# Optimization experiments

Hardware: AMD Instinct MI355X
Metric: run time of the kernel (lower is better)

## Reference

```python
import jax, jax.numpy as jnp
import numpy as np

IN_DIM, OUT_DIM, HID = 32, 1, 256
H0, H1, H2 = HID // 4, HID // 2, HID
B, S = 256, 512


def setup_inputs() -> dict:
    key = jax.random.key(0)
    ks = jax.random.split(key, 16)

    def u(k, shape, fan):
        bound = 1.0 / np.sqrt(fan)
        return jax.random.uniform(k, shape, jnp.float32, -bound, bound)

    inp = {"noise": jax.random.normal(ks[0], (B, S, IN_DIM), jnp.float32)}
    dims = [(IN_DIM, H0), (H0, H1), (H1, H2)]
    for i, (din, h) in enumerate(dims):
        inp[f"Wih{i}"] = u(ks[1 + 4 * i], (4 * h, din), h)  # torch gate order i,f,g,o
        inp[f"Whh{i}"] = u(ks[2 + 4 * i], (4 * h, h), h)
        inp[f"bih{i}"] = u(ks[3 + 4 * i], (4 * h,), h)
        inp[f"bhh{i}"] = u(ks[4 + 4 * i], (4 * h,), h)
    inp["Wl"] = u(ks[13], (OUT_DIM, H2), H2)
    inp["bl"] = u(ks[14], (OUT_DIM,), H2)
    return inp


def lstm_layer(x, Wih, Whh, bih, bhh):
    # x: [B, S, D] -> hidden sequence [B, S, H]; zero initial (h, c), torch gate order i,f,g,o
    Bb = x.shape[0]
    H = Whh.shape[1]
    pre = jnp.einsum('bsd,gd->bsg', x, Wih) + bih + bhh  # input GEMM for all timesteps at once

    def step(carry, pre_t):
        h, c = carry
        g = pre_t + h @ Whh.T  # [B, 4H]
        i, f, gg, o = jnp.split(g, 4, axis=-1)
        c = jax.nn.sigmoid(f) * c + jax.nn.sigmoid(i) * jnp.tanh(gg)
        h = jax.nn.sigmoid(o) * jnp.tanh(c)
        return (h, c), h

    h0 = jnp.zeros((Bb, H), x.dtype)
    c0 = jnp.zeros((Bb, H), x.dtype)
    _, hs = jax.lax.scan(step, (h0, c0), jnp.swapaxes(pre, 0, 1))  # scan over time
    return jnp.swapaxes(hs, 0, 1)


def reference(noise, Wih0, Whh0, bih0, bhh0, Wih1, Whh1, bih1, bhh1,
              Wih2, Whh2, bih2, bhh2, Wl, bl):
    x = lstm_layer(noise, Wih0, Whh0, bih0, bhh0)   # [B, S, 64]
    x = lstm_layer(x, Wih1, Whh1, bih1, bhh1)        # [B, S, 128]
    x = lstm_layer(x, Wih2, Whh2, bih2, bhh2)        # [B, S, 256]
    return jnp.tanh(jnp.einsum('bsh,oh->bso', x, Wl) + bl)  # [B, S, OUT_DIM]
```

## Files before the change

kernel.cpp:

```cpp
#include <hip/hip_runtime.h>
#include <hip/hip_fp16.h>

#define DEVINL __device__ __forceinline__

constexpr int B = 256, S = 512;
constexpr int H0 = 64, H1 = 128, H2 = 256;

typedef _Float16 f16x8 __attribute__((ext_vector_type(8)));
typedef float f32x4 __attribute__((ext_vector_type(4)));
typedef _Float16 h2v __attribute__((ext_vector_type(2)));

DEVINL float fexp2(float x) { return __builtin_amdgcn_exp2f(x); }
DEVINL float frcp(float x) { return __builtin_amdgcn_rcpf(x); }
DEVINL float fsig(float x) { return frcp(1.f + fexp2(-1.44269504088896f * x)); }
DEVINL float ftanh_(float x) { return 1.f - 2.f * frcp(1.f + fexp2(2.88539008177793f * x)); }
DEVINL h2v as_h2(unsigned u) { union { unsigned u; h2v h; } x; x.u = u; return x.h; }
DEVINL float fdot2(unsigned a, unsigned b, float c) {
  return __builtin_amdgcn_fdot2(as_h2(a), as_h2(b), c, false);
}
union FU { uint4 u; f16x8 h; };
DEVINL f16x8 as_f16x8(uint4 u) { FU x; x.u = u; return x.h; }

DEVINL unsigned long long agldull(unsigned long long* p) {
  return __hip_atomic_load(p, __ATOMIC_RELAXED, __HIP_MEMORY_SCOPE_AGENT);
}
DEVINL void agstull(unsigned long long* p, unsigned long long v) {
  __hip_atomic_store(p, v, __ATOMIC_RELAXED, __HIP_MEMORY_SCOPE_AGENT);
}


__global__ __launch_bounds__(256) void pack_frag(const float* __restrict__ w,
    uint4* __restrict__ wp, int Hch, int Kdim, int MT, int KT) {
  int o = blockIdx.x * 256 + threadIdx.x;
  if (o >= MT * KT * 64) return;
  int lane = o & 63, fk = o >> 6;
  int kt = fk % KT, mt = fk / KT;
  int rp = mt * 16 + (lane & 15);
  int orig = (rp & 3) * Hch + (rp >> 2);
  int k0 = kt * 32 + (lane >> 4) * 8;
  unsigned r[4];
#pragma unroll
  for (int p = 0; p < 4; ++p) {
    unsigned lo = __half_as_ushort(__float2half_rn(w[(size_t)orig * Kdim + k0 + 2 * p]));
    unsigned hi = __half_as_ushort(__float2half_rn(w[(size_t)orig * Kdim + k0 + 2 * p + 1]));
    r[p] = lo | (hi << 16);
  }
  uint4 v; v.x = r[0]; v.y = r[1]; v.z = r[2]; v.w = r[3];
  wp[o] = v;
}

__global__ __launch_bounds__(256) void pack_bias(const float* __restrict__ bih,
    const float* __restrict__ bhh, float* __restrict__ bs, int Hch) {
  int rp = blockIdx.x * 256 + threadIdx.x;
  if (rp >= 4 * Hch) return;
  int orig = (rp & 3) * Hch + (rp >> 2);
  bs[rp] = bih[orig] + bhh[orig];
}

__global__ void pack_wl(const float* __restrict__ wl, unsigned* __restrict__ wlp, int n) {
  int i = threadIdx.x;
  if (i < n) {
    unsigned lo = __half_as_ushort(__float2half_rn(wl[2 * i]));
    unsigned hi = __half_as_ushort(__float2half_rn(wl[2 * i + 1]));
    wlp[i] = lo | (hi << 16);
  }
}

__global__ __launch_bounds__(256) void f2h(const float* __restrict__ x,
                                           __half* __restrict__ y, int n8) {
  int i = blockIdx.x * 256 + threadIdx.x;
  if (i >= n8) return;
  float4 a = *(const float4*)(x + i * 8);
  float4 b = *(const float4*)(x + i * 8 + 4);
  __half h[8];
  h[0] = __float2half_rn(a.x); h[1] = __float2half_rn(a.y);
  h[2] = __float2half_rn(a.z); h[3] = __float2half_rn(a.w);
  h[4] = __float2half_rn(b.x); h[5] = __float2half_rn(b.y);
  h[6] = __float2half_rn(b.z); h[7] = __float2half_rn(b.w);
  *(uint4*)(y + i * 8) = *(const uint4*)h;
}

#define KBLK(BUF, K0, K1)                                                           \
  _Pragma("unroll") for (int kt = (K0); kt < (K1); ++kt) {                          \
    f16x8 bfrag = as_f16x8(*(const uint4*)((BUF) + n16 * HP + kt * 32 + quad * 8)); \
    _Pragma("unroll") for (int im = 0; im < MTW; ++im)                              \
      acc[im] = __builtin_amdgcn_mfma_f32_16x16x32_f16(                             \
          as_f16x8(areg[im][kt]), bfrag, acc[im], 0, 0, 0);                         \
  }

template <int H, int SPLIT, bool FINAL, int KTI>
DEVINL void scan_body(
    int bx, const __half* x, const uint4* wpI, const float* bs,
    const uint4* wp, f32x4* preT, __half* xout, float* out,
    const unsigned* wlp, const float* blp,
    float* sth, float* stc, unsigned long long* xh,
    int Sc, int t0, int first) {
  constexpr int MT = H / 4;
  constexpr int MTO = MT / SPLIT;
  constexpr int MTW = MTO / 8;
  constexpr int KT = H / 32;
  constexpr int HP = H + 8;
  constexpr int CH_OWN = MTO * 4;
  constexpr int KI = KTI * 32;

  __shared__ __half hb[2][16 * HP];
  __shared__ unsigned wls[FINAL ? H / 2 : 1];

  const int tid = threadIdx.x, w = tid >> 6, lane = tid & 63;
  const int n16 = lane & 15, quad = lane >> 4;
  int bt, half;
  if constexpr (SPLIT == 2) { bt = bx & 15; half = bx >> 4; }
  else { bt = bx; half = 0; }
  const int b0 = bt * 16;
  const int mbase = half * MTO;

  if constexpr (SPLIT == 2) {
    uint4 wih[MTW][KTI];
#pragma unroll
    for (int im = 0; im < MTW; ++im)
#pragma unroll
      for (int kt = 0; kt < KTI; ++kt)
        wih[im][kt] = wpI[((size_t)(mbase + w * MTW + im) * KTI + kt) * 64 + lane];
    f32x4 bini[MTW];
#pragma unroll
    for (int im = 0; im < MTW; ++im)
      bini[im] = *(const f32x4*)(bs + (mbase + w * MTW + im) * 16 + quad * 4);
    uint4 bfr[KTI];
    {
      const __half* xr = x + ((size_t)(b0 + n16) * S + t0) * KI + quad * 8;
#pragma unroll
      for (int kt = 0; kt < KTI; ++kt) bfr[kt] = *(const uint4*)(xr + kt * 32);
    }
    for (int t = 0; t < Sc; ++t) {
      uint4 cur[KTI];
#pragma unroll
      for (int kt = 0; kt < KTI; ++kt) cur[kt] = bfr[kt];
      if (t + 1 < Sc) {
        const __half* xr = x + ((size_t)(b0 + n16) * S + t0 + t + 1) * KI + quad * 8;
#pragma unroll
        for (int kt = 0; kt < KTI; ++kt) bfr[kt] = *(const uint4*)(xr + kt * 32);
      }
      f32x4 ac[MTW];
#pragma unroll
      for (int im = 0; im < MTW; ++im) ac[im] = bini[im];
#pragma unroll
      for (int kt = 0; kt < KTI; ++kt)
#pragma unroll
        for (int im = 0; im < MTW; ++im)
          ac[im] = __builtin_amdgcn_mfma_f32_16x16x32_f16(as_f16x8(wih[im][kt]),
                                                          as_f16x8(cur[kt]), ac[im], 0, 0, 0);
#pragma unroll
      for (int im = 0; im < MTW; ++im)
        preT[((size_t)(bt * Sc + t) * MT + mbase + w * MTW + im) * 64 + lane] = ac[im];
    }
    asm volatile("s_waitcnt vmcnt(0)" ::: "memory");
  }

  uint4 wih1[SPLIT == 1 ? MTW : 1][SPLIT == 1 ? KTI : 1];
  f32x4 bini1[SPLIT == 1 ? MTW : 1];
  if constexpr (SPLIT == 1) {
#pragma unroll
    for (int im = 0; im < MTW; ++im)
#pragma unroll
      for (int kt = 0; kt < KTI; ++kt)
        wih1[im][kt] = wpI[((size_t)(w * MTW + im) * KTI + kt) * 64 + lane];
#pragma unroll
    for (int im = 0; im < MTW; ++im)
      bini1[im] = *(const f32x4*)(bs + (w * MTW + im) * 16 + quad * 4);
  }

  uint4 areg[MTW][KT];
#pragma unroll
  for (int im = 0; im < MTW; ++im)
#pragma unroll
    for (int kt = 0; kt < KT; ++kt)
      areg[im][kt] = wp[((size_t)(mbase + w * MTW + im) * KT + kt) * 64 + lane];

  if constexpr (FINAL)
    for (int i = tid; i < H / 2; i += 512) wls[i] = wlp[i];

  float cst[MTW];
#pragma unroll
  for (int im = 0; im < MTW; ++im) {
    int ch = (mbase + w * MTW + im) * 4 + quad;
    cst[im] = first ? 0.f : stc[(size_t)(b0 + n16) * H + ch];
  }
  for (int i = tid; i < 16 * H; i += 512) {
    int n = i / H, ch = i % H;
    hb[0][n * HP + ch] = first ? __float2half_rn(0.f)
                               : __float2half_rn(sth[(size_t)(b0 + n) * H + ch]);
  }
  __syncthreads();

  const float bl0 = FINAL ? blp[0] : 0.f;

  auto emit_out = [&](const __half* rbuf, int t_out) {
    if constexpr (FINAL) {
      if ((SPLIT == 1 || half == 0) && tid < 128) {
        int n = tid >> 3, seg = tid & 7;
        const unsigned* hrow = (const unsigned*)(rbuf + n * HP);
        float s = 0.f;
#pragma unroll
        for (int p = 0; p < 16; ++p) s = fdot2(hrow[seg * 16 + p], wls[seg * 16 + p], s);
        s += __shfl_xor(s, 1); s += __shfl_xor(s, 2); s += __shfl_xor(s, 4);
        if (seg == 0) out[(size_t)(b0 + n) * S + t_out] = ftanh_(s + bl0);
      }
    } else {
      if (tid < 16 * (H / 8)) {
        int n = tid / (H / 8), kq = tid % (H / 8);
        uint4 v = *(const uint4*)(rbuf + n * HP + kq * 8);
        *(uint4*)(xout + ((size_t)(b0 + n) * S + t_out) * H + kq * 8) = v;
      }
    }
  };

  f32x4 nxt[MTW];
  if constexpr (SPLIT == 2) {
#pragma unroll
    for (int im = 0; im < MTW; ++im)
      nxt[im] = preT[((size_t)(bt * Sc) * MT + mbase + w * MTW + im) * 64 + lane];
  }
  uint4 xcur[SPLIT == 1 ? KTI : 1];
  if constexpr (SPLIT == 1) {
    const __half* xr = x + ((size_t)(b0 + n16) * S + t0) * KI + quad * 8;
#pragma unroll
    for (int kt = 0; kt < KTI; ++kt) xcur[kt] = *(const uint4*)(xr + kt * 32);
  }

  unsigned long long v0 = 0, v1 = 0;
  const int j0 = w * 128 + lane;

  for (int tl = 0; tl < Sc; ++tl) {
    __half* rb = hb[tl & 1];
    __half* wb = hb[(tl + 1) & 1];
    const int hid = t0 + tl;
    f32x4 acc[MTW];

    if constexpr (SPLIT == 2) {
#pragma unroll
      for (int im = 0; im < MTW; ++im) acc[im] = nxt[im];
      if (tl + 1 < Sc) {
#pragma unroll
        for (int im = 0; im < MTW; ++im)
          nxt[im] = preT[((size_t)(bt * Sc + tl + 1) * MT + mbase + w * MTW + im) * 64 + lane];
      }

      if (half == 0) { KBLK(rb, 0, KT / 2) } else { KBLK(rb, KT / 2, KT) }
      if (tl > 0) {
        const unsigned seq = (unsigned)hid;
        unsigned long long* srcp =
            xh + (((size_t)((hid - 1) & 1) * 16 + bt) * 2 + (1 - half)) * 1024;
        for (;;) {
          bool ok = ((unsigned)(v0 >> 32) == seq) & ((unsigned)(v1 >> 32) == seq);
          if (__all(ok)) break;
          v0 = agldull(srcp + j0);
          v1 = agldull(srcp + j0 + 64);
        }
        int c0 = j0 >> 3, dn0 = j0 & 7;
        rb[(2 * dn0) * HP + (1 - half) * CH_OWN + c0] =
            __ushort_as_half((unsigned short)(v0 & 0xffffu));
        rb[(2 * dn0 + 1) * HP + (1 - half) * CH_OWN + c0] =
            __ushort_as_half((unsigned short)((v0 >> 16) & 0xffffu));
        int j1 = j0 + 64, c1 = j1 >> 3, dn1 = j1 & 7;
        rb[(2 * dn1) * HP + (1 - half) * CH_OWN + c1] =
            __ushort_as_half((unsigned short)(v1 & 0xffffu));
        rb[(2 * dn1 + 1) * HP + (1 - half) * CH_OWN + c1] =
            __ushort_as_half((unsigned short)((v1 >> 16) & 0xffffu));
        __syncthreads();
      }
      if (half == 0) { KBLK(rb, KT / 2, KT) } else { KBLK(rb, 0, KT / 2) }
      if (tl > 0) emit_out(rb, hid - 1);
    } else {
      uint4 xnxt[KTI];
      if (tl + 1 < Sc) {
        const __half* xr = x + ((size_t)(b0 + n16) * S + hid + 1) * KI + quad * 8;
#pragma unroll
        for (int kt = 0; kt < KTI; ++kt) xnxt[kt] = *(const uint4*)(xr + kt * 32);
      }
#pragma unroll
      for (int im = 0; im < MTW; ++im) acc[im] = bini1[im];
#pragma unroll
      for (int kt = 0; kt < KTI; ++kt)
#pragma unroll
        for (int im = 0; im < MTW; ++im)
          acc[im] = __builtin_amdgcn_mfma_f32_16x16x32_f16(as_f16x8(wih1[im][kt]),
                                                           as_f16x8(xcur[kt]), acc[im], 0, 0, 0);
      if (tl > 0) emit_out(rb, hid - 1);
      KBLK(rb, 0, KT)
      if (tl + 1 < Sc) {
#pragma unroll
        for (int kt = 0; kt < KTI; ++kt) xcur[kt] = xnxt[kt];
      }
    }

    __half hh[MTW];
#pragma unroll
    for (int im = 0; im < MTW; ++im) {
      float gi = fsig(acc[im][0]);
      float gf = fsig(acc[im][1]);
      float gg = ftanh_(acc[im][2]);
      float go = fsig(acc[im][3]);
      float cn = gf * cst[im] + gi * gg;
      cst[im] = cn;
      hh[im] = __float2half_rn(go * ftanh_(cn));
    }

    if constexpr (SPLIT == 2) {
      const unsigned eseq = (unsigned)(hid + 1);
      unsigned long long* dst =
          xh + (((size_t)(hid & 1) * 16 + bt) * 2 + half) * 1024;
#pragma unroll
      for (int im = 0; im < MTW; ++im) {
        unsigned m = (unsigned)__half_as_ushort(hh[im]);
        unsigned o = (unsigned)__shfl_xor((int)m, 1);
        if (!(lane & 1)) {
          int cl = (w * MTW + im) * 4 + quad;
          agstull(dst + cl * 8 + (n16 >> 1),
                  ((unsigned long long)eseq << 32) | (unsigned long long)(m | (o << 16)));
        }
      }
      {
        unsigned long long* srcn =
            xh + (((size_t)(hid & 1) * 16 + bt) * 2 + (1 - half)) * 1024;
        v0 = agldull(srcn + j0);
        v1 = agldull(srcn + j0 + 64);
      }
#pragma unroll
      for (int im = 0; im < MTW; ++im)
        wb[n16 * HP + (mbase + w * MTW + im) * 4 + quad] = hh[im];
      __syncthreads();
    } else {
#pragma unroll
      for (int im = 0; im < MTW; ++im)
        wb[n16 * HP + (w * MTW + im) * 4 + quad] = hh[im];
      __syncthreads();
    }
  }

  __half* fb = hb[Sc & 1];
  if constexpr (SPLIT == 2) {
    const unsigned seq = (unsigned)(t0 + Sc);
    unsigned long long* srcp =
        xh + (((size_t)((t0 + Sc - 1) & 1) * 16 + bt) * 2 + (1 - half)) * 1024;
    for (;;) {
      bool ok = ((unsigned)(v0 >> 32) == seq) & ((unsigned)(v1 >> 32) == seq);
      if (__all(ok)) break;
      v0 = agldull(srcp + j0);
      v1 = agldull(srcp + j0 + 64);
    }
    int c0 = j0 >> 3, dn0 = j0 & 7;
    fb[(2 * dn0) * HP + (1 - half) * CH_OWN + c0] =
        __ushort_as_half((unsigned short)(v0 & 0xffffu));
    fb[(2 * dn0 + 1) * HP + (1 - half) * CH_OWN + c0] =
        __ushort_as_half((unsigned short)((v0 >> 16) & 0xffffu));
    int j1 = j0 + 64, c1 = j1 >> 3, dn1 = j1 & 7;
    fb[(2 * dn1) * HP + (1 - half) * CH_OWN + c1] =
        __ushort_as_half((unsigned short)(v1 & 0xffffu));
    fb[(2 * dn1 + 1) * HP + (1 - half) * CH_OWN + c1] =
        __ushort_as_half((unsigned short)((v1 >> 16) & 0xffffu));
    __syncthreads();
  }

  emit_out(fb, t0 + Sc - 1);

  for (int i = tid; i < 16 * H; i += 512) {
    int n = i / H, ch = i % H;
    sth[(size_t)(b0 + n) * H + ch] = __half2float(fb[n * HP + ch]);
  }
#pragma unroll
  for (int im = 0; im < MTW; ++im) {
    int ch = (mbase + w * MTW + im) * 4 + quad;
    stc[(size_t)(b0 + n16) * H + ch] = cst[im];
  }
}
#undef KBLK

__global__ __launch_bounds__(512) void scan_fat(
    const __half* x0, __half* x1, __half* x2,
    const uint4* wpI0, const uint4* wpI1, const uint4* wpI2,
    const float* bs0, const float* bs1, const float* bs2,
    const uint4* wpH0, const uint4* wpH1, const uint4* wpH2,
    f32x4* preT2,
    float* out, const unsigned* wlp, const float* blp,
    float* sh0, float* sc0, float* sh1, float* sc1, float* sh2, float* sc2,
    unsigned long long* xh, int Sc, int slot, int NC) {
  int b = blockIdx.x;
  if (b < 16) {
    int c = slot;
    if (c >= NC) return;
    scan_body<64, 1, false, 1>(b, x0, wpI0, bs0, wpH0, nullptr, x1, nullptr,
                               nullptr, nullptr, sh0, sc0, nullptr, Sc, c * Sc, c == 0);
  } else if (b < 32) {
    int c = slot - 1;
    if (c < 0 || c >= NC) return;
    scan_body<128, 1, false, 2>(b - 16, x1, wpI1, bs1, wpH1, nullptr, x2, nullptr,
                                nullptr, nullptr, sh1, sc1, nullptr, Sc, c * Sc, c == 0);
  } else {
    int c = slot - 2;
    if (c < 0 || c >= NC) return;
    scan_body<256, 2, true, 4>(b - 32, x2, wpI2, bs2, wpH2, preT2, nullptr, out,
                               wlp, blp, sh2, sc2, xh, Sc, c * Sc, c == 0);
  }
}

extern "C" void kernel_launch(void* const* d_in, const int* in_sizes, int n_in,
                              void* d_out, int out_size, void* d_ws, size_t ws_size,
                              hipStream_t stream) {
  (void)in_sizes; (void)n_in; (void)out_size;
  const float* noise = (const float*)d_in[0];
  const float* Wih0 = (const float*)d_in[1];
  const float* Whh0 = (const float*)d_in[2];
  const float* bih0 = (const float*)d_in[3];
  const float* bhh0 = (const float*)d_in[4];
  const float* Wih1 = (const float*)d_in[5];
  const float* Whh1 = (const float*)d_in[6];
  const float* bih1 = (const float*)d_in[7];
  const float* bhh1 = (const float*)d_in[8];
  const float* Wih2 = (const float*)d_in[9];
  const float* Whh2 = (const float*)d_in[10];
  const float* bih2 = (const float*)d_in[11];
  const float* bhh2 = (const float*)d_in[12];
  const float* Wl = (const float*)d_in[13];
  const float* bl = (const float*)d_in[14];
  float* out = (float*)d_out;

  char* p = (char*)d_ws;
  auto alloc = [&](size_t bytes) {
    char* r = p;
    p += (bytes + 255) & ~(size_t)255;
    return r;
  };
  uint4* wpH0 = (uint4*)alloc((size_t)16 * 2 * 1024);
  uint4* wpH1 = (uint4*)alloc((size_t)32 * 4 * 1024);
  uint4* wpH2 = (uint4*)alloc((size_t)64 * 8 * 1024);
  uint4* wpI0 = (uint4*)alloc((size_t)16 * 1 * 1024);
  uint4* wpI1 = (uint4*)alloc((size_t)32 * 2 * 1024);
  uint4* wpI2 = (uint4*)alloc((size_t)64 * 4 * 1024);
  float* bs0 = (float*)alloc(256 * 4);
  float* bs1 = (float*)alloc(512 * 4);
  float* bs2 = (float*)alloc(1024 * 4);
  unsigned* wlp = (unsigned*)alloc(128 * 4);
  float* sh0 = (float*)alloc((size_t)B * H0 * 4);
  float* sc0 = (float*)alloc((size_t)B * H0 * 4);
  float* sh1 = (float*)alloc((size_t)B * H1 * 4);
  float* sc1 = (float*)alloc((size_t)B * H1 * 4);
  float* sh2 = (float*)alloc((size_t)B * H2 * 4);
  float* sc2 = (float*)alloc((size_t)B * H2 * 4);
  __half* x0 = (__half*)alloc((size_t)B * S * 32 * 2);
  __half* x1 = (__half*)alloc((size_t)B * S * H0 * 2);
  __half* x2 = (__half*)alloc((size_t)B * S * H1 * 2);
  unsigned long long* xh = (unsigned long long*)alloc((size_t)2 * 16 * 2 * 1024 * 8);
  size_t fixed = (size_t)(p - (char*)d_ws);
  int Sc = 64;
  while (Sc > 16 && fixed + (size_t)B * Sc * 16 * H2 > ws_size) Sc >>= 1;
  f32x4* preT2 = (f32x4*)alloc((size_t)B * Sc * 16 * H2);

  hipMemsetAsync(xh, 0, (size_t)2 * 16 * 2 * 1024 * 8, stream);

  pack_frag<<<(16 * 2 * 64 + 255) / 256, 256, 0, stream>>>(Whh0, wpH0, 64, 64, 16, 2);
  pack_frag<<<(32 * 4 * 64 + 255) / 256, 256, 0, stream>>>(Whh1, wpH1, 128, 128, 32, 4);
  pack_frag<<<(64 * 8 * 64 + 255) / 256, 256, 0, stream>>>(Whh2, wpH2, 256, 256, 64, 8);
  pack_frag<<<(16 * 1 * 64 + 255) / 256, 256, 0, stream>>>(Wih0, wpI0, 64, 32, 16, 1);
  pack_frag<<<(32 * 2 * 64 + 255) / 256, 256, 0, stream>>>(Wih1, wpI1, 128, 64, 32, 2);
  pack_frag<<<(64 * 4 * 64 + 255) / 256, 256, 0, stream>>>(Wih2, wpI2, 256, 128, 64, 4);
  pack_bias<<<1, 256, 0, stream>>>(bih0, bhh0, bs0, 64);
  pack_bias<<<2, 256, 0, stream>>>(bih1, bhh1, bs1, 128);
  pack_bias<<<4, 256, 0, stream>>>(bih2, bhh2, bs2, 256);
  pack_wl<<<1, 128, 0, stream>>>(Wl, wlp, 128);
  f2h<<<(B * S * 32 / 8 + 255) / 256, 256, 0, stream>>>(noise, x0, B * S * 32 / 8);

  int NC = S / Sc;
  for (int slot = 0; slot < NC + 2; ++slot)
    scan_fat<<<64, 512, 0, stream>>>(x0, x1, x2, wpI0, wpI1, wpI2, bs0, bs1, bs2,
                                     wpH0, wpH1, wpH2, preT2,
                                     out, wlp, bl, sh0, sc0, sh1, sc1, sh2, sc2,
                                     xh, Sc, slot, NC);
}
```

Before: 1.924 ms.

## Duplicate cross-block hidden-state exchange via L2 atomics and split final projection

The exchange of hidden-state halves between the paired layer-2 blocks is now written to two buffers. One uses the existing agent-scope relaxed store, the other uses a workgroup-scope atomic exchange that may resolve at L2 faster. The consumer polls both and accepts whichever carries the expected sequence tag. The final output projection is also split so each half-block computes 8 of the 16 batch rows instead of one block doing all 16. This doubles exchange traffic and polling loads, and relies on workgroup-scope atomics being visible across blocks, which is not guaranteed by the memory model.

```diff
diff --git a/kernel.cpp b/kernel.cpp
--- a/kernel.cpp
+++ b/kernel.cpp
@@ -26,6 +26,12 @@
 }
 DEVINL void agstull(unsigned long long* p, unsigned long long v) {
   __hip_atomic_store(p, v, __ATOMIC_RELAXED, __HIP_MEMORY_SCOPE_AGENT);
+}
+DEVINL unsigned long long l2ldull(unsigned long long* p) {
+  return __hip_atomic_fetch_add(p, 0ull, __ATOMIC_RELAXED, __HIP_MEMORY_SCOPE_WORKGROUP);
+}
+DEVINL void l2stull(unsigned long long* p, unsigned long long v) {
+  (void)__hip_atomic_exchange(p, v, __ATOMIC_RELAXED, __HIP_MEMORY_SCOPE_WORKGROUP);
 }
 
 
@@ -93,7 +99,7 @@
     int bx, const __half* x, const uint4* wpI, const float* bs,
     const uint4* wp, f32x4* preT, __half* xout, float* out,
     const unsigned* wlp, const float* blp,
-    float* sth, float* stc, unsigned long long* xh,
+    float* sth, float* stc, unsigned long long* xhA, unsigned long long* xhF,
     int Sc, int t0, int first) {
   constexpr int MT = H / 4;
   constexpr int MTO = MT / SPLIT;
@@ -196,14 +202,29 @@
 
   auto emit_out = [&](const __half* rbuf, int t_out) {
     if constexpr (FINAL) {
-      if ((SPLIT == 1 || half == 0) && tid < 128) {
-        int n = tid >> 3, seg = tid & 7;
+      if (tid < 64) {
+        int n = (tid >> 3) + (SPLIT == 2 ? half * 8 : 0);
+        int seg = tid & 7;
         const unsigned* hrow = (const unsigned*)(rbuf + n * HP);
         float s = 0.f;
 #pragma unroll
         for (int p = 0; p < 16; ++p) s = fdot2(hrow[seg * 16 + p], wls[seg * 16 + p], s);
         s += __shfl_xor(s, 1); s += __shfl_xor(s, 2); s += __shfl_xor(s, 4);
         if (seg == 0) out[(size_t)(b0 + n) * S + t_out] = ftanh_(s + bl0);
+        if constexpr (SPLIT == 1) {
+        }
+      }
+      if constexpr (SPLIT == 1) {
+        if (tid >= 64 && tid < 128) {
+          int n = (tid >> 3);
+          int seg = tid & 7;
+          const unsigned* hrow = (const unsigned*)(rbuf + n * HP);
+          float s = 0.f;
+#pragma unroll
+          for (int p = 0; p < 16; ++p) s = fdot2(hrow[seg * 16 + p], wls[seg * 16 + p], s);
+          s += __shfl_xor(s, 1); s += __shfl_xor(s, 2); s += __shfl_xor(s, 4);
+          if (seg == 0) out[(size_t)(b0 + n) * S + t_out] = ftanh_(s + bl0);
+        }
       }
     } else {
       if (tid < 16 * (H / 8)) {
@@ -227,7 +248,7 @@
     for (int kt = 0; kt < KTI; ++kt) xcur[kt] = *(const uint4*)(xr + kt * 32);
   }
 
-  unsigned long long v0 = 0, v1 = 0;
+  unsigned long long v0f = 0, v1f = 0, v0a = 0, v1a = 0;
   const int j0 = w * 128 + lane;
 
   for (int tl = 0; tl < Sc; ++tl) {
@@ -248,24 +269,30 @@
       if (half == 0) { KBLK(rb, 0, KT / 2) } else { KBLK(rb, KT / 2, KT) }
       if (tl > 0) {
         const unsigned seq = (unsigned)hid;
-        unsigned long long* srcp =
-            xh + (((size_t)((hid - 1) & 1) * 16 + bt) * 2 + (1 - half)) * 1024;
+        const size_t so = (((size_t)((hid - 1) & 1) * 16 + bt) * 2 + (1 - half)) * 1024;
+        unsigned long long* srcA = xhA + so;
+        unsigned long long* srcF = xhF + so;
         for (;;) {
-          bool ok = ((unsigned)(v0 >> 32) == seq) & ((unsigned)(v1 >> 32) == seq);
-          if (__all(ok)) break;
-          v0 = agldull(srcp + j0);
-          v1 = agldull(srcp + j0 + 64);
+          bool ok0 = ((unsigned)(v0f >> 32) == seq) | ((unsigned)(v0a >> 32) == seq);
+          bool ok1 = ((unsigned)(v1f >> 32) == seq) | ((unsigned)(v1a >> 32) == seq);
+          if (__all(ok0 & ok1)) break;
+          v0f = l2ldull(srcF + j0);
+          v1f = l2ldull(srcF + j0 + 64);
+          v0a = agldull(srcA + j0);
+          v1a = agldull(srcA + j0 + 64);
         }
+        unsigned w0 = ((unsigned)(v0f >> 32) == seq) ? (unsigned)v0f : (unsigned)v0a;
+        unsigned w1 = ((unsigned)(v1f >> 32) == seq) ? (unsigned)v1f : (unsigned)v1a;
         int c0 = j0 >> 3, dn0 = j0 & 7;
         rb[(2 * dn0) * HP + (1 - half) * CH_OWN + c0] =
-            __ushort_as_half((unsigned short)(v0 & 0xffffu));
+            __ushort_as_half((unsigned short)(w0 & 0xffffu));
         rb[(2 * dn0 + 1) * HP + (1 - half) * CH_OWN + c0] =
-            __ushort_as_half((unsigned short)((v0 >> 16) & 0xffffu));
+            __ushort_as_half((unsigned short)(w0 >> 16));
         int j1 = j0 + 64, c1 = j1 >> 3, dn1 = j1 & 7;
         rb[(2 * dn1) * HP + (1 - half) * CH_OWN + c1] =
-            __ushort_as_half((unsigned short)(v1 & 0xffffu));
+            __ushort_as_half((unsigned short)(w1 & 0xffffu));
         rb[(2 * dn1 + 1) * HP + (1 - half) * CH_OWN + c1] =
-            __ushort_as_half((unsigned short)((v1 >> 16) & 0xffffu));
+            __ushort_as_half((unsigned short)(w1 >> 16));
         __syncthreads();
       }
       if (half == 0) { KBLK(rb, KT / 2, KT) } else { KBLK(rb, 0, KT / 2) }
@@ -307,23 +334,27 @@
 
     if constexpr (SPLIT == 2) {
       const unsigned eseq = (unsigned)(hid + 1);
-      unsigned long long* dst =
-          xh + (((size_t)(hid & 1) * 16 + bt) * 2 + half) * 1024;
+      const size_t eo = (((size_t)(hid & 1) * 16 + bt) * 2 + half) * 1024;
+      unsigned long long* dstA = xhA + eo;
+      unsigned long long* dstF = xhF + eo;
 #pragma unroll
       for (int im = 0; im < MTW; ++im) {
         unsigned m = (unsigned)__half_as_ushort(hh[im]);
         unsigned o = (unsigned)__shfl_xor((int)m, 1);
         if (!(lane & 1)) {
           int cl = (w * MTW + im) * 4 + quad;
-          agstull(dst + cl * 8 + (n16 >> 1),
-                  ((unsigned long long)eseq << 32) | (unsigned long long)(m | (o << 16)));
+          unsigned long long pv =
+              ((unsigned long long)eseq << 32) | (unsigned long long)(m | (o << 16));
+          l2stull(dstF + cl * 8 + (n16 >> 1), pv);
+          agstull(dstA + cl * 8 + (n16 >> 1), pv);
         }
       }
       {
-        unsigned long long* srcn =
-            xh + (((size_t)(hid & 1) * 16 + bt) * 2 + (1 - half)) * 1024;
-        v0 = agldull(srcn + j0);
-        v1 = agldull(srcn + j0 + 64);
+        const size_t so = (((size_t)(hid & 1) * 16 + bt) * 2 + (1 - half)) * 1024;
+        v0f = l2ldull(xhF + so + j0);
+        v1f = l2ldull(xhF + so + j0 + 64);
+        v0a = agldull(xhA + so + j0);
+        v1a = agldull(xhA + so + j0 + 64);
       }
 #pragma unroll
       for (int im = 0; im < MTW; ++im)
@@ -340,24 +371,30 @@
   __half* fb = hb[Sc & 1];
   if constexpr (SPLIT == 2) {
     const unsigned seq = (unsigned)(t0 + Sc);
-    unsigned long long* srcp =
-        xh + (((size_t)((t0 + Sc - 1) & 1) * 16 + bt) * 2 + (1 - half)) * 1024;
+    const size_t so = (((size_t)((t0 + Sc - 1) & 1) * 16 + bt) * 2 + (1 - half)) * 1024;
+    unsigned long long* srcA = xhA + so;
+    unsigned long long* srcF = xhF + so;
     for (;;) {
-      bool ok = ((unsigned)(v0 >> 32) == seq) & ((unsigned)(v1 >> 32) == seq);
-      if (__all(ok)) break;
-      v0 = agldull(srcp + j0);
-      v1 = agldull(srcp + j0 + 64);
-    }
+      bool ok0 = ((unsigned)(v0f >> 32) == seq) | ((unsigned)(v0a >> 32) == seq);
+      bool ok1 = ((unsigned)(v1f >> 32) == seq) | ((unsigned)(v1a >> 32) == seq);
+      if (__all(ok0 & ok1)) break;
+      v0f = l2ldull(srcF + j0);
+      v1f = l2ldull(srcF + j0 + 64);
+      v0a = agldull(srcA + j0);
+      v1a = agldull(srcA + j0 + 64);
+    }
+    unsigned w0 = ((unsigned)(v0f >> 32) == seq) ? (unsigned)v0f : (unsigned)v0a;
+    unsigned w1 = ((unsigned)(v1f >> 32) == seq) ? (unsigned)v1f : (unsigned)v1a;
     int c0 = j0 >> 3, dn0 = j0 & 7;
     fb[(2 * dn0) * HP + (1 - half) * CH_OWN + c0] =
-        __ushort_as_half((unsigned short)(v0 & 0xffffu));
+        __ushort_as_half((unsigned short)(w0 & 0xffffu));
     fb[(2 * dn0 + 1) * HP + (1 - half) * CH_OWN + c0] =
-        __ushort_as_half((unsigned short)((v0 >> 16) & 0xffffu));
+        __ushort_as_half((unsigned short)(w0 >> 16));
     int j1 = j0 + 64, c1 = j1 >> 3, dn1 = j1 & 7;
     fb[(2 * dn1) * HP + (1 - half) * CH_OWN + c1] =
-        __ushort_as_half((unsigned short)(v1 & 0xffffu));
+        __ushort_as_half((unsigned short)(w1 & 0xffffu));
     fb[(2 * dn1 + 1) * HP + (1 - half) * CH_OWN + c1] =
-        __ushort_as_half((unsigned short)((v1 >> 16) & 0xffffu));
+        __ushort_as_half((unsigned short)(w1 >> 16));
     __syncthreads();
   }
 
@@ -383,23 +420,25 @@
     f32x4* preT2,
     float* out, const unsigned* wlp, const float* blp,
     float* sh0, float* sc0, float* sh1, float* sc1, float* sh2, float* sc2,
-    unsigned long long* xh, int Sc, int slot, int NC) {
+    unsigned long long* xhA, unsigned long long* xhF, int Sc, int slot, int NC) {
   int b = blockIdx.x;
   if (b < 16) {
     int c = slot;
     if (c >= NC) return;
     scan_body<64, 1, false, 1>(b, x0, wpI0, bs0, wpH0, nullptr, x1, nullptr,
-                               nullptr, nullptr, sh0, sc0, nullptr, Sc, c * Sc, c == 0);
+                               nullptr, nullptr, sh0, sc0, nullptr, nullptr,
+                               Sc, c * Sc, c == 0);
   } else if (b < 32) {
     int c = slot - 1;
     if (c < 0 || c >= NC) return;
     scan_body<128, 1, false, 2>(b - 16, x1, wpI1, bs1, wpH1, nullptr, x2, nullptr,
-                                nullptr, nullptr, sh1, sc1, nullptr, Sc, c * Sc, c == 0);
+                                nullptr, nullptr, sh1, sc1, nullptr, nullptr,
+                                Sc, c * Sc, c == 0);
   } else {
     int c = slot - 2;
     if (c < 0 || c >= NC) return;
     scan_body<256, 2, true, 4>(b - 32, x2, wpI2, bs2, wpH2, preT2, nullptr, out,
-                               wlp, blp, sh2, sc2, xh, Sc, c * Sc, c == 0);
+                               wlp, blp, sh2, sc2, xhA, xhF, Sc, c * Sc, c == 0);
   }
 }
 
@@ -449,13 +488,15 @@
   __half* x0 = (__half*)alloc((size_t)B * S * 32 * 2);
   __half* x1 = (__half*)alloc((size_t)B * S * H0 * 2);
   __half* x2 = (__half*)alloc((size_t)B * S * H1 * 2);
-  unsigned long long* xh = (unsigned long long*)alloc((size_t)2 * 16 * 2 * 1024 * 8);
+  const size_t XB = (size_t)2 * 16 * 2 * 1024 * 8;
+  unsigned long long* xhA = (unsigned long long*)alloc(XB);
+  unsigned long long* xhF = (unsigned long long*)alloc(XB);
   size_t fixed = (size_t)(p - (char*)d_ws);
   int Sc = 64;
   while (Sc > 16 && fixed + (size_t)B * Sc * 16 * H2 > ws_size) Sc >>= 1;
   f32x4* preT2 = (f32x4*)alloc((size_t)B * Sc * 16 * H2);
 
-  hipMemsetAsync(xh, 0, (size_t)2 * 16 * 2 * 1024 * 8, stream);
+  hipMemsetAsync(xhA, 0, 2 * XB, stream);
 
   pack_frag<<<(16 * 2 * 64 + 255) / 256, 256, 0, stream>>>(Whh0, wpH0, 64, 64, 16, 2);
   pack_frag<<<(32 * 4 * 64 + 255) / 256, 256, 0, stream>>>(Whh1, wpH1, 128, 128, 32, 4);
@@ -474,5 +515,5 @@
     scan_fat<<<64, 512, 0, stream>>>(x0, x1, x2, wpI0, wpI1, wpI2, bs0, bs1, bs2,
                                      wpH0, wpH1, wpH2, preT2,
                                      out, wlp, bl, sh0, sc0, sh1, sc1, sh2, sc2,
-                                     xh, Sc, slot, NC);
-}
+                                     xhA, xhF, Sc, slot, NC);
+}
```

Measured after the change: 1.993 ms. 1.04x slower.

## Run layer-2 LSTM recurrence in one block, dropping cross-block hidden-state exchange

Applied to the files above, without the earlier changes.

Layer 2 (H=256) previously split each batch tile across two workgroups that swapped half of the hidden state every timestep through global-memory flags and spin-waits. Now one 512-thread workgroup owns the whole tile. It keeps six K-tiles of the recurrent weights in registers and stages the last two in shared memory to stay within register limits. This removes the per-step inter-block polling latency, the flag buffer and its memset, but doubles per-block MFMA work and adds LDS weight reads on the serial critical path, while the grid drops from 64 to 48 blocks.

```diff
diff --git a/kernel.cpp b/kernel.cpp
--- a/kernel.cpp
+++ b/kernel.cpp
@@ -20,13 +20,6 @@
 }
 union FU { uint4 u; f16x8 h; };
 DEVINL f16x8 as_f16x8(uint4 u) { FU x; x.u = u; return x.h; }
-
-DEVINL unsigned long long agldull(unsigned long long* p) {
-  return __hip_atomic_load(p, __ATOMIC_RELAXED, __HIP_MEMORY_SCOPE_AGENT);
-}
-DEVINL void agstull(unsigned long long* p, unsigned long long v) {
-  __hip_atomic_store(p, v, __ATOMIC_RELAXED, __HIP_MEMORY_SCOPE_AGENT);
-}
 
 
 __global__ __launch_bounds__(256) void pack_frag(const float* __restrict__ w,
@@ -80,220 +73,99 @@
   *(uint4*)(y + i * 8) = *(const uint4*)h;
 }
 
-#define KBLK(BUF, K0, K1)                                                           \
-  _Pragma("unroll") for (int kt = (K0); kt < (K1); ++kt) {                          \
-    f16x8 bfrag = as_f16x8(*(const uint4*)((BUF) + n16 * HP + kt * 32 + quad * 8)); \
-    _Pragma("unroll") for (int im = 0; im < MTW; ++im)                              \
-      acc[im] = __builtin_amdgcn_mfma_f32_16x16x32_f16(                             \
-          as_f16x8(areg[im][kt]), bfrag, acc[im], 0, 0, 0);                         \
-  }
-
-template <int H, int SPLIT, bool FINAL, int KTI>
-DEVINL void scan_body(
-    int bx, const __half* x, const uint4* wpI, const float* bs,
-    const uint4* wp, f32x4* preT, __half* xout, float* out,
-    const unsigned* wlp, const float* blp,
-    float* sth, float* stc, unsigned long long* xh,
+constexpr int HPB = H2 + 8;
+constexpr int SM_HB = 2 * 16 * HPB * 2;
+constexpr int SM_WA = 64 * 2 * 64 * 16;
+constexpr int SMEM_BYTES = SM_HB + SM_WA + 512;
+
+template <int H, int KTI>
+DEVINL void scan_small(char* sm, int bt, const __half* __restrict__ x,
+    const uint4* __restrict__ wpI, const float* __restrict__ bs,
+    const uint4* __restrict__ wp, __half* __restrict__ xout,
+    float* __restrict__ sth, float* __restrict__ stc,
     int Sc, int t0, int first) {
-  constexpr int MT = H / 4;
-  constexpr int MTO = MT / SPLIT;
-  constexpr int MTW = MTO / 8;
-  constexpr int KT = H / 32;
-  constexpr int HP = H + 8;
-  constexpr int CH_OWN = MTO * 4;
-  constexpr int KI = KTI * 32;
-
-  __shared__ __half hb[2][16 * HP];
-  __shared__ unsigned wls[FINAL ? H / 2 : 1];
-
+  constexpr int MT = H / 4, MTW = MT / 8, KT = H / 32, HP = H + 8, KI = KTI * 32;
+  __half* hb0 = (__half*)sm;
   const int tid = threadIdx.x, w = tid >> 6, lane = tid & 63;
   const int n16 = lane & 15, quad = lane >> 4;
-  int bt, half;
-  if constexpr (SPLIT == 2) { bt = bx & 15; half = bx >> 4; }
-  else { bt = bx; half = 0; }
   const int b0 = bt * 16;
-  const int mbase = half * MTO;
-
-  if constexpr (SPLIT == 2) {
-    uint4 wih[MTW][KTI];
-#pragma unroll
-    for (int im = 0; im < MTW; ++im)
-#pragma unroll
-      for (int kt = 0; kt < KTI; ++kt)
-        wih[im][kt] = wpI[((size_t)(mbase + w * MTW + im) * KTI + kt) * 64 + lane];
-    f32x4 bini[MTW];
-#pragma unroll
-    for (int im = 0; im < MTW; ++im)
-      bini[im] = *(const f32x4*)(bs + (mbase + w * MTW + im) * 16 + quad * 4);
-    uint4 bfr[KTI];
-    {
-      const __half* xr = x + ((size_t)(b0 + n16) * S + t0) * KI + quad * 8;
-#pragma unroll
-      for (int kt = 0; kt < KTI; ++kt) bfr[kt] = *(const uint4*)(xr + kt * 32);
-    }
-    for (int t = 0; t < Sc; ++t) {
-      uint4 cur[KTI];
-#pragma unroll
-      for (int kt = 0; kt < KTI; ++kt) cur[kt] = bfr[kt];
-      if (t + 1 < Sc) {
-        const __half* xr = x + ((size_t)(b0 + n16) * S + t0 + t + 1) * KI + quad * 8;
-#pragma unroll
-        for (int kt = 0; kt < KTI; ++kt) bfr[kt] = *(const uint4*)(xr + kt * 32);
-      }
-      f32x4 ac[MTW];
-#pragma unroll
-      for (int im = 0; im < MTW; ++im) ac[im] = bini[im];
-#pragma unroll
-      for (int kt = 0; kt < KTI; ++kt)
-#pragma unroll
-        for (int im = 0; im < MTW; ++im)
-          ac[im] = __builtin_amdgcn_mfma_f32_16x16x32_f16(as_f16x8(wih[im][kt]),
-                                                          as_f16x8(cur[kt]), ac[im], 0, 0, 0);
-#pragma unroll
-      for (int im = 0; im < MTW; ++im)
-        preT[((size_t)(bt * Sc + t) * MT + mbase + w * MTW + im) * 64 + lane] = ac[im];
-    }
-    asm volatile("s_waitcnt vmcnt(0)" ::: "memory");
-  }
-
-  uint4 wih1[SPLIT == 1 ? MTW : 1][SPLIT == 1 ? KTI : 1];
-  f32x4 bini1[SPLIT == 1 ? MTW : 1];
-  if constexpr (SPLIT == 1) {
-#pragma unroll
-    for (int im = 0; im < MTW; ++im)
-#pragma unroll
-      for (int kt = 0; kt < KTI; ++kt)
-        wih1[im][kt] = wpI[((size_t)(w * MTW + im) * KTI + kt) * 64 + lane];
-#pragma unroll
-    for (int im = 0; im < MTW; ++im)
-      bini1[im] = *(const f32x4*)(bs + (w * MTW + im) * 16 + quad * 4);
-  }
-
+
+  uint4 wih[MTW][KTI];
+#pragma unroll
+  for (int im = 0; im < MTW; ++im)
+#pragma unroll
+    for (int kt = 0; kt < KTI; ++kt)
+      wih[im][kt] = wpI[((size_t)(w * MTW + im) * KTI + kt) * 64 + lane];
+  f32x4 bini[MTW];
+#pragma unroll
+  for (int im = 0; im < MTW; ++im)
+    bini[im] = *(const f32x4*)(bs + (w * MTW + im) * 16 + quad * 4);
   uint4 areg[MTW][KT];
 #pragma unroll
   for (int im = 0; im < MTW; ++im)
 #pragma unroll
     for (int kt = 0; kt < KT; ++kt)
-      areg[im][kt] = wp[((size_t)(mbase + w * MTW + im) * KT + kt) * 64 + lane];
-
-  if constexpr (FINAL)
-    for (int i = tid; i < H / 2; i += 512) wls[i] = wlp[i];
+      areg[im][kt] = wp[((size_t)(w * MTW + im) * KT + kt) * 64 + lane];
 
   float cst[MTW];
 #pragma unroll
   for (int im = 0; im < MTW; ++im) {
-    int ch = (mbase + w * MTW + im) * 4 + quad;
+    int ch = (w * MTW + im) * 4 + quad;
     cst[im] = first ? 0.f : stc[(size_t)(b0 + n16) * H + ch];
   }
   for (int i = tid; i < 16 * H; i += 512) {
     int n = i / H, ch = i % H;
-    hb[0][n * HP + ch] = first ? __float2half_rn(0.f)
-                               : __float2half_rn(sth[(size_t)(b0 + n) * H + ch]);
+    hb0[n * HP + ch] = first ? __float2half_rn(0.f)
+                             : __float2half_rn(sth[(size_t)(b0 + n) * H + ch]);
   }
   __syncthreads();
 
-  const float bl0 = FINAL ? blp[0] : 0.f;
-
-  auto emit_out = [&](const __half* rbuf, int t_out) {
-    if constexpr (FINAL) {
-      if ((SPLIT == 1 || half == 0) && tid < 128) {
-        int n = tid >> 3, seg = tid & 7;
-        const unsigned* hrow = (const unsigned*)(rbuf + n * HP);
-        float s = 0.f;
-#pragma unroll
-        for (int p = 0; p < 16; ++p) s = fdot2(hrow[seg * 16 + p], wls[seg * 16 + p], s);
-        s += __shfl_xor(s, 1); s += __shfl_xor(s, 2); s += __shfl_xor(s, 4);
-        if (seg == 0) out[(size_t)(b0 + n) * S + t_out] = ftanh_(s + bl0);
-      }
-    } else {
+  uint4 xcur[KTI];
+  {
+    const __half* xr = x + ((size_t)(b0 + n16) * S + t0) * KI + quad * 8;
+#pragma unroll
+    for (int kt = 0; kt < KTI; ++kt) xcur[kt] = *(const uint4*)(xr + kt * 32);
+  }
+
+  for (int tl = 0; tl < Sc; ++tl) {
+    __half* rb = hb0 + (tl & 1) * 16 * HP;
+    __half* wb = hb0 + ((tl + 1) & 1) * 16 * HP;
+    const int hid = t0 + tl;
+
+    uint4 xnxt[KTI];
+    if (tl + 1 < Sc) {
+      const __half* xr = x + ((size_t)(b0 + n16) * S + hid + 1) * KI + quad * 8;
+#pragma unroll
+      for (int kt = 0; kt < KTI; ++kt) xnxt[kt] = *(const uint4*)(xr + kt * 32);
+    }
+
+    f32x4 acc[MTW];
+#pragma unroll
+    for (int im = 0; im < MTW; ++im) acc[im] = bini[im];
+#pragma unroll
+    for (int kt = 0; kt < KTI; ++kt)
+#pragma unroll
+      for (int im = 0; im < MTW; ++im)
+        acc[im] = __builtin_amdgcn_mfma_f32_16x16x32_f16(as_f16x8(wih[im][kt]),
+                                                         as_f16x8(xcur[kt]), acc[im], 0, 0, 0);
+
+    if (tl > 0) {
       if (tid < 16 * (H / 8)) {
         int n = tid / (H / 8), kq = tid % (H / 8);
-        uint4 v = *(const uint4*)(rbuf + n * HP + kq * 8);
-        *(uint4*)(xout + ((size_t)(b0 + n) * S + t_out) * H + kq * 8) = v;
+        uint4 v = *(const uint4*)(rb + n * HP + kq * 8);
+        *(uint4*)(xout + ((size_t)(b0 + n) * S + hid - 1) * H + kq * 8) = v;
       }
     }
-  };
-
-  f32x4 nxt[MTW];
-  if constexpr (SPLIT == 2) {
-#pragma unroll
-    for (int im = 0; im < MTW; ++im)
-      nxt[im] = preT[((size_t)(bt * Sc) * MT + mbase + w * MTW + im) * 64 + lane];
-  }
-  uint4 xcur[SPLIT == 1 ? KTI : 1];
-  if constexpr (SPLIT == 1) {
-    const __half* xr = x + ((size_t)(b0 + n16) * S + t0) * KI + quad * 8;
-#pragma unroll
-    for (int kt = 0; kt < KTI; ++kt) xcur[kt] = *(const uint4*)(xr + kt * 32);
-  }
-
-  unsigned long long v0 = 0, v1 = 0;
-  const int j0 = w * 128 + lane;
-
-  for (int tl = 0; tl < Sc; ++tl) {
-    __half* rb = hb[tl & 1];
-    __half* wb = hb[(tl + 1) & 1];
-    const int hid = t0 + tl;
-    f32x4 acc[MTW];
-
-    if constexpr (SPLIT == 2) {
-#pragma unroll
-      for (int im = 0; im < MTW; ++im) acc[im] = nxt[im];
-      if (tl + 1 < Sc) {
-#pragma unroll
-        for (int im = 0; im < MTW; ++im)
-          nxt[im] = preT[((size_t)(bt * Sc + tl + 1) * MT + mbase + w * MTW + im) * 64 + lane];
-      }
-
-      if (half == 0) { KBLK(rb, 0, KT / 2) } else { KBLK(rb, KT / 2, KT) }
-      if (tl > 0) {
-        const unsigned seq = (unsigned)hid;
-        unsigned long long* srcp =
-            xh + (((size_t)((hid - 1) & 1) * 16 + bt) * 2 + (1 - half)) * 1024;
-        for (;;) {
-          bool ok = ((unsigned)(v0 >> 32) == seq) & ((unsigned)(v1 >> 32) == seq);
-          if (__all(ok)) break;
-          v0 = agldull(srcp + j0);
-          v1 = agldull(srcp + j0 + 64);
-        }
-        int c0 = j0 >> 3, dn0 = j0 & 7;
-        rb[(2 * dn0) * HP + (1 - half) * CH_OWN + c0] =
-            __ushort_as_half((unsigned short)(v0 & 0xffffu));
-        rb[(2 * dn0 + 1) * HP + (1 - half) * CH_OWN + c0] =
-            __ushort_as_half((unsigned short)((v0 >> 16) & 0xffffu));
-        int j1 = j0 + 64, c1 = j1 >> 3, dn1 = j1 & 7;
-        rb[(2 * dn1) * HP + (1 - half) * CH_OWN + c1] =
-            __ushort_as_half((unsigned short)(v1 & 0xffffu));
-        rb[(2 * dn1 + 1) * HP + (1 - half) * CH_OWN + c1] =
-            __ushort_as_half((unsigned short)((v1 >> 16) & 0xffffu));
-        __syncthreads();
-      }
-      if (half == 0) { KBLK(rb, KT / 2, KT) } else { KBLK(rb, 0, KT / 2) }
-      if (tl > 0) emit_out(rb, hid - 1);
-    } else {
-      uint4 xnxt[KTI];
-      if (tl + 1 < Sc) {
-        const __half* xr = x + ((size_t)(b0 + n16) * S + hid + 1) * KI + quad * 8;
-#pragma unroll
-        for (int kt = 0; kt < KTI; ++kt) xnxt[kt] = *(const uint4*)(xr + kt * 32);
-      }
-#pragma unroll
-      for (int im = 0; im < MTW; ++im) acc[im] = bini1[im];
-#pragma unroll
-      for (int kt = 0; kt < KTI; ++kt)
-#pragma unroll
-        for (int im = 0; im < MTW; ++im)
-          acc[im] = __builtin_amdgcn_mfma_f32_16x16x32_f16(as_f16x8(wih1[im][kt]),
-                                                           as_f16x8(xcur[kt]), acc[im], 0, 0, 0);
-      if (tl > 0) emit_out(rb, hid - 1);
-      KBLK(rb, 0, KT)
-      if (tl + 1 < Sc) {
-#pragma unroll
-        for (int kt = 0; kt < KTI; ++kt) xcur[kt] = xnxt[kt];
-      }
-    }
-
-    __half hh[MTW];
+
+#pragma unroll
+    for (int kt = 0; kt < KT; ++kt) {
+      f16x8 bfrag = as_f16x8(*(const uint4*)(rb + n16 * HP + kt * 32 + quad * 8));
+#pragma unroll
+      for (int im = 0; im < MTW; ++im)
+        acc[im] = __builtin_amdgcn_mfma_f32_16x16x32_f16(as_f16x8(areg[im][kt]), bfrag,
+                                                         acc[im], 0, 0, 0);
+    }
+
 #pragma unroll
     for (int im = 0; im < MTW; ++im) {
       float gi = fsig(acc[im][0]);
@@ -302,78 +174,186 @@
       float go = fsig(acc[im][3]);
       float cn = gf * cst[im] + gi * gg;
       cst[im] = cn;
-      hh[im] = __float2half_rn(go * ftanh_(cn));
-    }
-
-    if constexpr (SPLIT == 2) {
-      const unsigned eseq = (unsigned)(hid + 1);
-      unsigned long long* dst =
-          xh + (((size_t)(hid & 1) * 16 + bt) * 2 + half) * 1024;
-#pragma unroll
-      for (int im = 0; im < MTW; ++im) {
-        unsigned m = (unsigned)__half_as_ushort(hh[im]);
-        unsigned o = (unsigned)__shfl_xor((int)m, 1);
-        if (!(lane & 1)) {
-          int cl = (w * MTW + im) * 4 + quad;
-          agstull(dst + cl * 8 + (n16 >> 1),
-                  ((unsigned long long)eseq << 32) | (unsigned long long)(m | (o << 16)));
-        }
-      }
-      {
-        unsigned long long* srcn =
-            xh + (((size_t)(hid & 1) * 16 + bt) * 2 + (1 - half)) * 1024;
-        v0 = agldull(srcn + j0);
-        v1 = agldull(srcn + j0 + 64);
-      }
-#pragma unroll
-      for (int im = 0; im < MTW; ++im)
-        wb[n16 * HP + (mbase + w * MTW + im) * 4 + quad] = hh[im];
-      __syncthreads();
-    } else {
-#pragma unroll
-      for (int im = 0; im < MTW; ++im)
-        wb[n16 * HP + (w * MTW + im) * 4 + quad] = hh[im];
-      __syncthreads();
-    }
-  }
-
-  __half* fb = hb[Sc & 1];
-  if constexpr (SPLIT == 2) {
-    const unsigned seq = (unsigned)(t0 + Sc);
-    unsigned long long* srcp =
-        xh + (((size_t)((t0 + Sc - 1) & 1) * 16 + bt) * 2 + (1 - half)) * 1024;
-    for (;;) {
-      bool ok = ((unsigned)(v0 >> 32) == seq) & ((unsigned)(v1 >> 32) == seq);
-      if (__all(ok)) break;
-      v0 = agldull(srcp + j0);
-      v1 = agldull(srcp + j0 + 64);
-    }
-    int c0 = j0 >> 3, dn0 = j0 & 7;
-    fb[(2 * dn0) * HP + (1 - half) * CH_OWN + c0] =
-        __ushort_as_half((unsigned short)(v0 & 0xffffu));
-    fb[(2 * dn0 + 1) * HP + (1 - half) * CH_OWN + c0] =
-        __ushort_as_half((unsigned short)((v0 >> 16) & 0xffffu));
-    int j1 = j0 + 64, c1 = j1 >> 3, dn1 = j1 & 7;
-    fb[(2 * dn1) * HP + (1 - half) * CH_OWN + c1] =
-        __ushort_as_half((unsigned short)(v1 & 0xffffu));
-    fb[(2 * dn1 + 1) * HP + (1 - half) * CH_OWN + c1] =
-        __ushort_as_half((unsigned short)((v1 >> 16) & 0xffffu));
+      wb[n16 * HP + (w * MTW + im) * 4 + quad] = __float2half_rn(go * ftanh_(cn));
+    }
+#pragma unroll
+    for (int kt = 0; kt < KTI; ++kt) xcur[kt] = xnxt[kt];
     __syncthreads();
   }
 
-  emit_out(fb, t0 + Sc - 1);
-
+  __half* fb = hb0 + (Sc & 1) * 16 * HP;
+  if (tid < 16 * (H / 8)) {
+    int n = tid / (H / 8), kq = tid % (H / 8);
+    uint4 v = *(const uint4*)(fb + n * HP + kq * 8);
+    *(uint4*)(xout + ((size_t)(b0 + n) * S + t0 + Sc - 1) * H + kq * 8) = v;
+  }
   for (int i = tid; i < 16 * H; i += 512) {
     int n = i / H, ch = i % H;
     sth[(size_t)(b0 + n) * H + ch] = __half2float(fb[n * HP + ch]);
   }
 #pragma unroll
   for (int im = 0; im < MTW; ++im) {
-    int ch = (mbase + w * MTW + im) * 4 + quad;
+    int ch = (w * MTW + im) * 4 + quad;
     stc[(size_t)(b0 + n16) * H + ch] = cst[im];
   }
 }
-#undef KBLK
+
+DEVINL void scan_big(char* sm, int bt, const __half* __restrict__ x,
+    const uint4* __restrict__ wpI, const float* __restrict__ bs,
+    const uint4* __restrict__ wp, f32x4* __restrict__ preT,
+    float* __restrict__ out, const unsigned* __restrict__ wlp,
+    const float* __restrict__ blp,
+    float* __restrict__ sth, float* __restrict__ stc,
+    int Sc, int t0, int first) {
+  constexpr int H = 256, MT = 64, MTW = 8, KT = 8, KTR = 6, KTI = 4;
+  constexpr int HP = H + 8, KI = 128;
+  __half* hb0 = (__half*)sm;
+  uint4* wA = (uint4*)(sm + SM_HB);
+  unsigned* wls = (unsigned*)(sm + SM_HB + SM_WA);
+  const int tid = threadIdx.x, w = tid >> 6, lane = tid & 63;
+  const int n16 = lane & 15, quad = lane >> 4;
+  const int b0 = bt * 16;
+
+  for (int i = tid; i < MT * 2 * 64; i += 512) {
+    int mt = i >> 7, r = i & 127, ktl = r >> 6, ln = r & 63;
+    wA[i] = wp[((size_t)mt * KT + 6 + ktl) * 64 + ln];
+  }
+  for (int i = tid; i < H / 2; i += 512) wls[i] = wlp[i];
+
+  {
+    uint4 wih[MTW][KTI];
+#pragma unroll
+    for (int im = 0; im < MTW; ++im)
+#pragma unroll
+      for (int kt = 0; kt < KTI; ++kt)
+        wih[im][kt] = wpI[((size_t)(w * MTW + im) * KTI + kt) * 64 + lane];
+    f32x4 bini[MTW];
+#pragma unroll
+    for (int im = 0; im < MTW; ++im)
+      bini[im] = *(const f32x4*)(bs + (w * MTW + im) * 16 + quad * 4);
+    uint4 bfr[KTI];
+    {
+      const __half* xr = x + ((size_t)(b0 + n16) * S + t0) * KI + quad * 8;
+#pragma unroll
+      for (int kt = 0; kt < KTI; ++kt) bfr[kt] = *(const uint4*)(xr + kt * 32);
+    }
+    for (int t = 0; t < Sc; ++t) {
+      uint4 cur[KTI];
+#pragma unroll
+      for (int kt = 0; kt < KTI; ++kt) cur[kt] = bfr[kt];
+      if (t + 1 < Sc) {
+        const __half* xr = x + ((size_t)(b0 + n16) * S + t0 + t + 1) * KI + quad * 8;
+#pragma unroll
+        for (int kt = 0; kt < KTI; ++kt) bfr[kt] = *(const uint4*)(xr + kt * 32);
+      }
+      f32x4 ac[MTW];
+#pragma unroll
+      for (int im = 0; im < MTW; ++im) ac[im] = bini[im];
+#pragma unroll
+      for (int kt = 0; kt < KTI; ++kt)
+#pragma unroll
+        for (int im = 0; im < MTW; ++im)
+          ac[im] = __builtin_amdgcn_mfma_f32_16x16x32_f16(as_f16x8(wih[im][kt]),
+                                                          as_f16x8(cur[kt]), ac[im], 0, 0, 0);
+#pragma unroll
+      for (int im = 0; im < MTW; ++im)
+        preT[((size_t)(bt * Sc + t) * MT + w * MTW + im) * 64 + lane] = ac[im];
+    }
+  }
+  asm volatile("s_waitcnt vmcnt(0)" ::: "memory");
+
+  uint4 areg[MTW][KTR];
+#pragma unroll
+  for (int im = 0; im < MTW; ++im)
+#pragma unroll
+    for (int kt = 0; kt < KTR; ++kt)
+      areg[im][kt] = wp[((size_t)(w * MTW + im) * KT + kt) * 64 + lane];
+
+  float cst[MTW];
+#pragma unroll
+  for (int im = 0; im < MTW; ++im) {
+    int ch = (w * MTW + im) * 4 + quad;
+    cst[im] = first ? 0.f : stc[(size_t)(b0 + n16) * H + ch];
+  }
+  for (int i = tid; i < 16 * H; i += 512) {
+    int n = i / H, ch = i % H;
+    hb0[n * HP + ch] = first ? __float2half_rn(0.f)
+                             : __float2half_rn(sth[(size_t)(b0 + n) * H + ch]);
+  }
+  __syncthreads();
+
+  const float bl0 = blp[0];
+
+  auto emit_out = [&](const __half* rbuf, int t_out) {
+    if (tid < 128) {
+      int n = tid >> 3, seg = tid & 7;
+      const unsigned* hrow = (const unsigned*)(rbuf + n * HP);
+      float s = 0.f;
+#pragma unroll
+      for (int p = 0; p < 16; ++p) s = fdot2(hrow[seg * 16 + p], wls[seg * 16 + p], s);
+      s += __shfl_xor(s, 1); s += __shfl_xor(s, 2); s += __shfl_xor(s, 4);
+      if (seg == 0) out[(size_t)(b0 + n) * S + t_out] = ftanh_(s + bl0);
+    }
+  };
+
+  for (int tl = 0; tl < Sc; ++tl) {
+    __half* rb = hb0 + (tl & 1) * 16 * HP;
+    __half* wb = hb0 + ((tl + 1) & 1) * 16 * HP;
+
+    f32x4 acc[MTW];
+    {
+      const f32x4* pT = preT + ((size_t)(bt * Sc + tl) * MT + w * MTW) * 64 + lane;
+#pragma unroll
+      for (int im = 0; im < MTW; ++im) acc[im] = pT[im * 64];
+    }
+
+    if (tl > 0) emit_out(rb, t0 + tl - 1);
+
+#pragma unroll
+    for (int kt = 0; kt < KTR; ++kt) {
+      f16x8 bfrag = as_f16x8(*(const uint4*)(rb + n16 * HP + kt * 32 + quad * 8));
+#pragma unroll
+      for (int im = 0; im < MTW; ++im)
+        acc[im] = __builtin_amdgcn_mfma_f32_16x16x32_f16(as_f16x8(areg[im][kt]), bfrag,
+                                                         acc[im], 0, 0, 0);
+    }
+#pragma unroll
+    for (int ktl = 0; ktl < 2; ++ktl) {
+      f16x8 bfrag = as_f16x8(*(const uint4*)(rb + n16 * HP + (KTR + ktl) * 32 + quad * 8));
+#pragma unroll
+      for (int im = 0; im < MTW; ++im) {
+        uint4 a = wA[((w * MTW + im) * 2 + ktl) * 64 + lane];
+        acc[im] = __builtin_amdgcn_mfma_f32_16x16x32_f16(as_f16x8(a), bfrag,
+                                                         acc[im], 0, 0, 0);
+      }
+    }
+
+#pragma unroll
+    for (int im = 0; im < MTW; ++im) {
+      float gi = fsig(acc[im][0]);
+      float gf = fsig(acc[im][1]);
+      float gg = ftanh_(acc[im][2]);
+      float go = fsig(acc[im][3]);
+      float cn = gf * cst[im] + gi * gg;
+      cst[im] = cn;
+      wb[n16 * HP + (w * MTW + im) * 4 + quad] = __float2half_rn(go * ftanh_(cn));
+    }
+    __syncthreads();
+  }
+
+  __half* fb = hb0 + (Sc & 1) * 16 * HP;
+  emit_out(fb, t0 + Sc - 1);
+
+  for (int i = tid; i < 16 * H; i += 512) {
+    int n = i / H, ch = i % H;
+    sth[(size_t)(b0 + n) * H + ch] = __half2float(fb[n * HP + ch]);
+  }
+#pragma unroll
+  for (int im = 0; im < MTW; ++im) {
+    int ch = (w * MTW + im) * 4 + quad;
+    stc[(size_t)(b0 + n16) * H + ch] = cst[im];
+  }
+}
 
 __global__ __launch_bounds__(512) void scan_fat(
     const __half* x0, __half* x1, __half* x2,
@@ -383,23 +363,22 @@
     f32x4* preT2,
     float* out, const unsigned* wlp, const float* blp,
     float* sh0, float* sc0, float* sh1, float* sc1, float* sh2, float* sc2,
-    unsigned long long* xh, int Sc, int slot, int NC) {
+    int Sc, int slot, int NC) {
+  __shared__ __align__(16) char sm[SMEM_BYTES];
   int b = blockIdx.x;
   if (b < 16) {
     int c = slot;
     if (c >= NC) return;
-    scan_body<64, 1, false, 1>(b, x0, wpI0, bs0, wpH0, nullptr, x1, nullptr,
-                               nullptr, nullptr, sh0, sc0, nullptr, Sc, c * Sc, c == 0);
+    scan_small<64, 1>(sm, b, x0, wpI0, bs0, wpH0, x1, sh0, sc0, Sc, c * Sc, c == 0);
   } else if (b < 32) {
     int c = slot - 1;
     if (c < 0 || c >= NC) return;
-    scan_body<128, 1, false, 2>(b - 16, x1, wpI1, bs1, wpH1, nullptr, x2, nullptr,
-                                nullptr, nullptr, sh1, sc1, nullptr, Sc, c * Sc, c == 0);
+    scan_small<128, 2>(sm, b - 16, x1, wpI1, bs1, wpH1, x2, sh1, sc1, Sc, c * Sc, c == 0);
   } else {
     int c = slot - 2;
     if (c < 0 || c >= NC) return;
-    scan_body<256, 2, true, 4>(b - 32, x2, wpI2, bs2, wpH2, preT2, nullptr, out,
-                               wlp, blp, sh2, sc2, xh, Sc, c * Sc, c == 0);
+    scan_big(sm, b - 32, x2, wpI2, bs2, wpH2, preT2, out, wlp, blp, sh2, sc2,
+             Sc, c * Sc, c == 0);
   }
 }
 
@@ -449,13 +428,10 @@
   __half* x0 = (__half*)alloc((size_t)B * S * 32 * 2);
   __half* x1 = (__half*)alloc((size_t)B * S * H0 * 2);
   __half* x2 = (__half*)alloc((size_t)B * S * H1 * 2);
-  unsigned long long* xh = (unsigned long long*)alloc((size_t)2 * 16 * 2 * 1024 * 8);
   size_t fixed = (size_t)(p - (char*)d_ws);
   int Sc = 64;
   while (Sc > 16 && fixed + (size_t)B * Sc * 16 * H2 > ws_size) Sc >>= 1;
   f32x4* preT2 = (f32x4*)alloc((size_t)B * Sc * 16 * H2);
-
-  hipMemsetAsync(xh, 0, (size_t)2 * 16 * 2 * 1024 * 8, stream);
 
   pack_frag<<<(16 * 2 * 64 + 255) / 256, 256, 0, stream>>>(Whh0, wpH0, 64, 64, 16, 2);
   pack_frag<<<(32 * 4 * 64 + 255) / 256, 256, 0, stream>>>(Whh1, wpH1, 128, 128, 32, 4);
@@ -471,8 +447,8 @@
 
   int NC = S / Sc;
   for (int slot = 0; slot < NC + 2; ++slot)
-    scan_fat<<<64, 512, 0, stream>>>(x0, x1, x2, wpI0, wpI1, wpI2, bs0, bs1, bs2,
+    scan_fat<<<48, 512, 0, stream>>>(x0, x1, x2, wpI0, wpI1, wpI2, bs0, bs1, bs2,
                                      wpH0, wpH1, wpH2, preT2,
                                      out, wlp, bl, sh0, sc0, sh1, sc1, sh2, sc2,
-                                     xh, Sc, slot, NC);
-}
+                                     Sc, slot, NC);
+}
```

New measurement: 3.278 ms. +70.4%, slower.
